# Kernel optimization log

Measured on AMD Instinct MI355X. Metric: run time of the kernel, lower is better.

## Reference

```python
import jax, jax.numpy as jnp
import numpy as np

B, N, D, E = 2, 50000, 64, 800000


def setup_inputs() -> dict:
    key = jax.random.key(0)
    k = jax.random.split(key, 6)
    return {
        "prev_embeddings": jax.random.normal(k[0], (B, N, D), dtype=jnp.float32),
        "edges_ij": jax.random.randint(k[1], (E, 2), 0, N, dtype=jnp.int64 if jax.config.jax_enable_x64 else jnp.int32),
        "node_features_embeddings": jax.random.normal(k[2], (B, N, D), dtype=jnp.float32),
        "edge_features_embeddings": jax.random.normal(k[3], (B, N, D), dtype=jnp.float32),
        "edge_status": jax.random.uniform(k[4], (E,), dtype=jnp.float32),
        "W": jax.random.normal(k[5], (D, D), dtype=jnp.float32) / np.sqrt(D).astype(np.float32),
    }


def reference(prev_embeddings, edges_ij, node_features_embeddings, edge_features_embeddings, edge_status, W):
    # prev_embeddings: (B, N, D); edges_ij: (E, 2); edge_status: (E,) in [0,1]; W: (D, D) theta2 weight (no bias)
    u = edges_ij[:, 0]
    v = edges_ij[:, 1]
    g = edge_status.astype(prev_embeddings.dtype).reshape(1, -1, 1)  # broadcast (1,E,1) over batch
    h_u = prev_embeddings[:, u, :] * g  # gather source endpoint, gate
    h_v = prev_embeddings[:, v, :] * g  # gather dest endpoint, gate
    # scatter-add gated messages in both directions: nbr[b, v] += h_u, nbr[b, u] += h_v
    nbr = jnp.zeros_like(prev_embeddings).at[:, v, :].add(h_u).at[:, u, :].add(h_v)
    x2 = jnp.einsum('bnd,ed->bne', nbr, W)  # Linear(D,D,bias=False): nbr @ W.T
    return jax.nn.leaky_relu(node_features_embeddings + x2 + edge_features_embeddings)
```

## Files before the change

kernel.cpp:

```cpp
#include <hip/hip_runtime.h>

constexpr int B = 2;
constexpr int N = 50000;
constexpr int D = 64;
constexpr int E = 800000;
constexpr int CAP = 96;
constexpr int XG = 8;
constexpr int NPG = N / XG;

__device__ __forceinline__ unsigned f2bf(float f) {
    unsigned u = __float_as_uint(f);
    return (u + 0x7FFFu + ((u >> 16) & 1u)) >> 16;
}
__device__ __forceinline__ float bfhi2f(unsigned bits) {
    return __uint_as_float(bits & 0xFFFF0000u);
}
__device__ __forceinline__ float bflo2f(unsigned bits) {
    return __uint_as_float(bits << 16);
}

__global__ __launch_bounds__(256) void convert_kernel(
    const float4* __restrict__ prev4, uint2* __restrict__ prevb)
{
    int i = blockIdx.x * 256 + threadIdx.x;
    float4 v = prev4[i];
    uint2 o;
    o.x = f2bf(v.x) | (f2bf(v.y) << 16);
    o.y = f2bf(v.z) | (f2bf(v.w) << 16);
    prevb[i] = o;
}

__global__ __launch_bounds__(256) void build_kernel(
    const int2* __restrict__ edges, const float* __restrict__ status,
    int* __restrict__ counts, unsigned* __restrict__ slots)
{
    int g = blockIdx.x & 7;
    int e = (blockIdx.x >> 3) * 256 + threadIdx.x;
    if (e >= E) return;
    int2 uv = edges[e];
    unsigned gb = f2bf(status[e]) << 16;
    if (uv.x / NPG == g) {
        int p = atomicAdd(&counts[uv.x], 1);
        if (p < CAP) slots[(size_t)uv.x * CAP + p] = gb | (unsigned)uv.y;
    }
    if (uv.y / NPG == g) {
        int p = atomicAdd(&counts[uv.y], 1);
        if (p < CAP) slots[(size_t)uv.y * CAP + p] = gb | (unsigned)uv.x;
    }
}

__global__ __launch_bounds__(256) void gather_fused(
    const uint2* __restrict__ prevb,
    const int* __restrict__ counts,
    const unsigned* __restrict__ slots,
    const float* __restrict__ node,
    const float* __restrict__ edgef,
    const float* __restrict__ W,
    float* __restrict__ out)
{
    __shared__ float Wl[D][D + 1];
    __shared__ float xs[4][2][D];

    int t = threadIdx.x;
    for (int i = t; i < D * D; i += 256) Wl[i >> 6][i & 63] = W[i];

    int wave = t >> 6, lane = t & 63;
    int n = blockIdx.x * 4 + wave;
    int q = lane & 15, sub = lane >> 4;

    int cnt = min(counts[n], CAP);
    size_t base = (size_t)n * CAP;
    const uint2* p0 = prevb;
    const uint2* p1 = prevb + (size_t)N * 16;

    float a00 = 0.f, a01 = 0.f, a02 = 0.f, a03 = 0.f;
    float a10 = 0.f, a11 = 0.f, a12 = 0.f, a13 = 0.f;

    for (int k = sub; k < cnt; k += 4) {
        unsigned ent = slots[base + k];
        float g = bfhi2f(ent);
        int nb = ent & 0xFFFF;
        uint2 r0 = p0[(size_t)nb * 16 + q];
        uint2 r1 = p1[(size_t)nb * 16 + q];
        a00 += g * bflo2f(r0.x); a01 += g * bfhi2f(r0.x);
        a02 += g * bflo2f(r0.y); a03 += g * bfhi2f(r0.y);
        a10 += g * bflo2f(r1.x); a11 += g * bfhi2f(r1.x);
        a12 += g * bflo2f(r1.y); a13 += g * bfhi2f(r1.y);
    }

    a00 += __shfl_xor(a00, 16, 64); a00 += __shfl_xor(a00, 32, 64);
    a01 += __shfl_xor(a01, 16, 64); a01 += __shfl_xor(a01, 32, 64);
    a02 += __shfl_xor(a02, 16, 64); a02 += __shfl_xor(a02, 32, 64);
    a03 += __shfl_xor(a03, 16, 64); a03 += __shfl_xor(a03, 32, 64);
    a10 += __shfl_xor(a10, 16, 64); a10 += __shfl_xor(a10, 32, 64);
    a11 += __shfl_xor(a11, 16, 64); a11 += __shfl_xor(a11, 32, 64);
    a12 += __shfl_xor(a12, 16, 64); a12 += __shfl_xor(a12, 32, 64);
    a13 += __shfl_xor(a13, 16, 64); a13 += __shfl_xor(a13, 32, 64);

    if (sub == 0) {
        *(float4*)&xs[wave][0][q * 4] = make_float4(a00, a01, a02, a03);
        *(float4*)&xs[wave][1][q * 4] = make_float4(a10, a11, a12, a13);
    }
    __syncthreads();

    float acc0 = 0.f, acc1 = 0.f;
#pragma unroll
    for (int d = 0; d < D; ++d) {
        float w = Wl[lane][d];
        acc0 += xs[wave][0][d] * w;
        acc1 += xs[wave][1][d] * w;
    }

    size_t b0 = (size_t)n * D + lane;
    size_t b1 = (size_t)N * D + b0;
    float y0 = node[b0] + acc0 + edgef[b0];
    float y1 = node[b1] + acc1 + edgef[b1];
    out[b0] = (y0 >= 0.f) ? y0 : 0.01f * y0;
    out[b1] = (y1 >= 0.f) ? y1 : 0.01f * y1;
}

__device__ inline void atomic_add4(float* p, float4 val, float g) {
    atomicAdd(p + 0, val.x * g);
    atomicAdd(p + 1, val.y * g);
    atomicAdd(p + 2, val.z * g);
    atomicAdd(p + 3, val.w * g);
}

__global__ __launch_bounds__(256) void scatter_kernel(
    const float* __restrict__ prev,
    const int2* __restrict__ edges,
    const float* __restrict__ status,
    float* __restrict__ nbr)
{
    int idx = blockIdx.x * 256 + threadIdx.x;
    int e = idx >> 4;
    int q = idx & 15;
    if (e >= E) return;
    int2 uv = edges[e];
    float g = status[e];
    const float4* p0 = (const float4*)prev;
    const float4* p1 = (const float4*)(prev + (size_t)N * D);
    float4 pu0 = p0[(size_t)uv.x * 16 + q];
    float4 pv0 = p0[(size_t)uv.y * 16 + q];
    float4 pu1 = p1[(size_t)uv.x * 16 + q];
    float4 pv1 = p1[(size_t)uv.y * 16 + q];
    float* n0 = nbr;
    float* n1 = nbr + (size_t)N * D;
    int off_v = uv.y * D + q * 4;
    int off_u = uv.x * D + q * 4;
    atomic_add4(n0 + off_v, pu0, g);
    atomic_add4(n0 + off_u, pv0, g);
    atomic_add4(n1 + off_v, pu1, g);
    atomic_add4(n1 + off_u, pv1, g);
}

__global__ __launch_bounds__(256) void gemm_relu_kernel(
    float* __restrict__ out,
    const float* __restrict__ node,
    const float* __restrict__ edgef,
    const float* __restrict__ W)
{
    __shared__ float Wl[D][D + 1];
    __shared__ float xs[4][D];
    int t = threadIdx.x;
    for (int i = t; i < D * D; i += 256) Wl[i >> 6][i & 63] = W[i];
    int wave = t >> 6, lane = t & 63;
    int row = blockIdx.x * 4 + wave;
    size_t base = (size_t)row * D;
    float x = out[base + lane];
    xs[wave][lane] = x;
    __syncthreads();
    float acc = 0.f;
#pragma unroll
    for (int d = 0; d < D; ++d) acc += xs[wave][d] * Wl[lane][d];
    float y = node[base + lane] + acc + edgef[base + lane];
    out[base + lane] = (y >= 0.f) ? y : 0.01f * y;
}

extern "C" void kernel_launch(void* const* d_in, const int* in_sizes, int n_in,
                              void* d_out, int out_size, void* d_ws, size_t ws_size,
                              hipStream_t stream) {
    const float* prev   = (const float*)d_in[0];
    const int*   edges  = (const int*)d_in[1];
    const float* node   = (const float*)d_in[2];
    const float* edgef  = (const float*)d_in[3];
    const float* status = (const float*)d_in[4];
    const float* W      = (const float*)d_in[5];
    float* out = (float*)d_out;

    const int2* edges2 = (const int2*)edges;

    size_t slots_bytes  = (size_t)N * CAP * sizeof(unsigned);
    size_t counts_bytes = (size_t)N * sizeof(int);
    size_t prevb_bytes  = (size_t)B * N * D * 2;
    size_t need = slots_bytes + counts_bytes + prevb_bytes;

    if (ws_size >= need) {
        unsigned* slots = (unsigned*)d_ws;
        int* counts = (int*)((char*)d_ws + slots_bytes);
        uint2* prevb = (uint2*)((char*)d_ws + slots_bytes + counts_bytes);

        hipMemsetAsync(counts, 0, counts_bytes, stream);
        convert_kernel<<<(B * N * D / 4) / 256, 256, 0, stream>>>(
            (const float4*)prev, prevb);
        build_kernel<<<(E / 256) * XG, 256, 0, stream>>>(
            edges2, status, counts, slots);
        gather_fused<<<N / 4, 256, 0, stream>>>(
            (const uint2*)prevb, counts, slots, node, edgef, W, out);
    } else {
        hipMemsetAsync(out, 0, (size_t)B * N * D * sizeof(float), stream);
        scatter_kernel<<<(E * 16) / 256, 256, 0, stream>>>(prev, edges2, status, out);
        gemm_relu_kernel<<<(B * N) / 4, 256, 0, stream>>>(out, node, edgef, W);
    }
}
```

Before: 303.1 us.

## Apply W before gathering and split gather by batch and half-row

Uses linearity to multiply prev by W first in a separate per-row GEMM kernel that writes bf16 results, then gathers the pre-transformed rows, so the fused gather no longer does the matvec. The gather grid is also split four ways by batch and half of the feature dimension, so each wave loads 4-byte pieces instead of two 8-byte pieces per neighbor. This raises block count for latency hiding, but the slot lists are now read four times and each gather touches smaller, less coalesced segments. Rounding now happens after the W multiply rather than before, which changes numerics slightly.

```diff
diff --git a/kernel.cpp b/kernel.cpp
--- a/kernel.cpp
+++ b/kernel.cpp
@@ -7,6 +7,7 @@
 constexpr int CAP = 96;
 constexpr int XG = 8;
 constexpr int NPG = N / XG;
+constexpr int GBLK = N / 4;
 
 __device__ __forceinline__ unsigned f2bf(float f) {
     unsigned u = __float_as_uint(f);
@@ -19,15 +20,31 @@
     return __uint_as_float(bits << 16);
 }
 
-__global__ __launch_bounds__(256) void convert_kernel(
-    const float4* __restrict__ prev4, uint2* __restrict__ prevb)
-{
-    int i = blockIdx.x * 256 + threadIdx.x;
-    float4 v = prev4[i];
-    uint2 o;
-    o.x = f2bf(v.x) | (f2bf(v.y) << 16);
-    o.y = f2bf(v.z) | (f2bf(v.w) << 16);
-    prevb[i] = o;
+__global__ __launch_bounds__(256) void pgemm_kernel(
+    const float* __restrict__ prev,
+    const float* __restrict__ W,
+    unsigned* __restrict__ P32)
+{
+    __shared__ float Wl[D][D + 1];
+    __shared__ float xs[4][D];
+
+    int t = threadIdx.x;
+    for (int i = t; i < D * D; i += 256) Wl[i >> 6][i & 63] = W[i];
+
+    int wave = t >> 6, lane = t & 63;
+    size_t row = (size_t)blockIdx.x * 4 + wave;
+
+    xs[wave][lane] = prev[row * D + lane];
+    __syncthreads();
+
+    float acc = 0.f;
+#pragma unroll
+    for (int d = 0; d < D; ++d) acc += xs[wave][d] * Wl[lane][d];
+
+    float partner = __shfl_xor(acc, 1, 64);
+    if ((lane & 1) == 0) {
+        P32[row * 32 + (lane >> 1)] = f2bf(acc) | (f2bf(partner) << 16);
+    }
 }
 
 __global__ __launch_bounds__(256) void build_kernel(
@@ -49,74 +66,48 @@
     }
 }
 
-__global__ __launch_bounds__(256) void gather_fused(
-    const uint2* __restrict__ prevb,
+__global__ __launch_bounds__(256) void gather_out(
+    const unsigned* __restrict__ P32,
     const int* __restrict__ counts,
     const unsigned* __restrict__ slots,
-    const float* __restrict__ node,
-    const float* __restrict__ edgef,
-    const float* __restrict__ W,
-    float* __restrict__ out)
-{
-    __shared__ float Wl[D][D + 1];
-    __shared__ float xs[4][2][D];
-
-    int t = threadIdx.x;
-    for (int i = t; i < D * D; i += 256) Wl[i >> 6][i & 63] = W[i];
-
-    int wave = t >> 6, lane = t & 63;
-    int n = blockIdx.x * 4 + wave;
+    const float2* __restrict__ node2,
+    const float2* __restrict__ edgef2,
+    float2* __restrict__ out2)
+{
+    int pid = blockIdx.x;
+    int phase = pid / GBLK;
+    int nblk = pid - phase * GBLK;
+    int b = phase >> 1, h = phase & 1;
+
+    int wave = threadIdx.x >> 6, lane = threadIdx.x & 63;
+    int n = nblk * 4 + wave;
     int q = lane & 15, sub = lane >> 4;
 
     int cnt = min(counts[n], CAP);
-    size_t base = (size_t)n * CAP;
-    const uint2* p0 = prevb;
-    const uint2* p1 = prevb + (size_t)N * 16;
-
-    float a00 = 0.f, a01 = 0.f, a02 = 0.f, a03 = 0.f;
-    float a10 = 0.f, a11 = 0.f, a12 = 0.f, a13 = 0.f;
-
+    size_t sbase = (size_t)n * CAP;
+    const unsigned* Pb = P32 + (size_t)b * N * 32 + 16 * h + q;
+
+    float a0 = 0.f, a1 = 0.f;
     for (int k = sub; k < cnt; k += 4) {
-        unsigned ent = slots[base + k];
+        unsigned ent = slots[sbase + k];
         float g = bfhi2f(ent);
-        int nb = ent & 0xFFFF;
-        uint2 r0 = p0[(size_t)nb * 16 + q];
-        uint2 r1 = p1[(size_t)nb * 16 + q];
-        a00 += g * bflo2f(r0.x); a01 += g * bfhi2f(r0.x);
-        a02 += g * bflo2f(r0.y); a03 += g * bfhi2f(r0.y);
-        a10 += g * bflo2f(r1.x); a11 += g * bfhi2f(r1.x);
-        a12 += g * bflo2f(r1.y); a13 += g * bfhi2f(r1.y);
-    }
-
-    a00 += __shfl_xor(a00, 16, 64); a00 += __shfl_xor(a00, 32, 64);
-    a01 += __shfl_xor(a01, 16, 64); a01 += __shfl_xor(a01, 32, 64);
-    a02 += __shfl_xor(a02, 16, 64); a02 += __shfl_xor(a02, 32, 64);
-    a03 += __shfl_xor(a03, 16, 64); a03 += __shfl_xor(a03, 32, 64);
-    a10 += __shfl_xor(a10, 16, 64); a10 += __shfl_xor(a10, 32, 64);
-    a11 += __shfl_xor(a11, 16, 64); a11 += __shfl_xor(a11, 32, 64);
-    a12 += __shfl_xor(a12, 16, 64); a12 += __shfl_xor(a12, 32, 64);
-    a13 += __shfl_xor(a13, 16, 64); a13 += __shfl_xor(a13, 32, 64);
+        unsigned nb = ent & 0xFFFFu;
+        unsigned r = Pb[(size_t)nb * 32];
+        a0 += g * bflo2f(r);
+        a1 += g * bfhi2f(r);
+    }
+
+    a0 += __shfl_xor(a0, 16, 64); a0 += __shfl_xor(a0, 32, 64);
+    a1 += __shfl_xor(a1, 16, 64); a1 += __shfl_xor(a1, 32, 64);
 
     if (sub == 0) {
-        *(float4*)&xs[wave][0][q * 4] = make_float4(a00, a01, a02, a03);
-        *(float4*)&xs[wave][1][q * 4] = make_float4(a10, a11, a12, a13);
-    }
-    __syncthreads();
-
-    float acc0 = 0.f, acc1 = 0.f;
-#pragma unroll
-    for (int d = 0; d < D; ++d) {
-        float w = Wl[lane][d];
-        acc0 += xs[wave][0][d] * w;
-        acc1 += xs[wave][1][d] * w;
-    }
-
-    size_t b0 = (size_t)n * D + lane;
-    size_t b1 = (size_t)N * D + b0;
-    float y0 = node[b0] + acc0 + edgef[b0];
-    float y1 = node[b1] + acc1 + edgef[b1];
-    out[b0] = (y0 >= 0.f) ? y0 : 0.01f * y0;
-    out[b1] = (y1 >= 0.f) ? y1 : 0.01f * y1;
+        size_t o = ((size_t)b * N + n) * 32 + 16 * h + q;
+        float2 nd = node2[o], ef = edgef2[o];
+        float y0 = nd.x + a0 + ef.x;
+        float y1 = nd.y + a1 + ef.y;
+        out2[o] = make_float2((y0 >= 0.f) ? y0 : 0.01f * y0,
+                              (y1 >= 0.f) ? y1 : 0.01f * y1);
+    }
 }
 
 __device__ inline void atomic_add4(float* p, float4 val, float g) {
@@ -192,21 +183,21 @@
 
     size_t slots_bytes  = (size_t)N * CAP * sizeof(unsigned);
     size_t counts_bytes = (size_t)N * sizeof(int);
-    size_t prevb_bytes  = (size_t)B * N * D * 2;
-    size_t need = slots_bytes + counts_bytes + prevb_bytes;
+    size_t p_bytes      = (size_t)B * N * 32 * sizeof(unsigned);
+    size_t need = slots_bytes + counts_bytes + p_bytes;
 
     if (ws_size >= need) {
         unsigned* slots = (unsigned*)d_ws;
         int* counts = (int*)((char*)d_ws + slots_bytes);
-        uint2* prevb = (uint2*)((char*)d_ws + slots_bytes + counts_bytes);
+        unsigned* P32 = (unsigned*)((char*)d_ws + slots_bytes + counts_bytes);
 
         hipMemsetAsync(counts, 0, counts_bytes, stream);
-        convert_kernel<<<(B * N * D / 4) / 256, 256, 0, stream>>>(
-            (const float4*)prev, prevb);
+        pgemm_kernel<<<(B * N) / 4, 256, 0, stream>>>(prev, W, P32);
         build_kernel<<<(E / 256) * XG, 256, 0, stream>>>(
             edges2, status, counts, slots);
-        gather_fused<<<N / 4, 256, 0, stream>>>(
-            (const uint2*)prevb, counts, slots, node, edgef, W, out);
+        gather_out<<<4 * GBLK, 256, 0, stream>>>(
+            P32, counts, slots, (const float2*)node, (const float2*)edgef,
+            (float2*)out);
     } else {
         hipMemsetAsync(out, 0, (size_t)B * N * D * sizeof(float), stream);
         scatter_kernel<<<(E * 16) / 256, 256, 0, stream>>>(prev, edges2, status, out);
```

Result: slower. 431.4 us (+42.3%).
